# Kernel tuning notes

Measured on AMD Instinct MI355X. Metric: run time of the kernel, lower is better.

The kernel has to match this reference:

```python
import jax, jax.numpy as jnp
import numpy as np

N_HEAD = 8
HID = 64
IN_DIM = 512
OUT_DIM = 512


def setup_inputs() -> dict:
    key = jax.random.key(0)
    ks = jax.random.split(key, 12)
    B, LQ, LK = 2, 2048, 2048
    stdv = 1.0 / np.sqrt(HID)
    inp = {
        "q": jax.random.normal(ks[0], (B, LQ, IN_DIM), jnp.float32),
        "k": jax.random.normal(ks[1], (B, LK, IN_DIM), jnp.float32),
        "v": jax.random.normal(ks[2], (B, LK, IN_DIM), jnp.float32),
        # linear params stored as (in, out); torch Linear applies x @ W.T + b,
        # we store pre-transposed weights so y = x @ W + b is the same math.
        "Wq": jax.random.normal(ks[3], (IN_DIM, N_HEAD * HID), jnp.float32) * 0.02,
        "bq": jnp.zeros((N_HEAD * HID,), jnp.float32),
        "Wk": jax.random.normal(ks[4], (IN_DIM, N_HEAD * HID), jnp.float32) * 0.02,
        "bk": jnp.zeros((N_HEAD * HID,), jnp.float32),
        "Wv": jax.random.normal(ks[5], (IN_DIM, N_HEAD * HID), jnp.float32) * 0.02,
        "bv": jnp.zeros((N_HEAD * HID,), jnp.float32),
        # mlp-method scoring vector, uniform(-stdv, stdv), length 2*hidden
        "w_score": jax.random.uniform(ks[6], (2 * HID,), jnp.float32, -stdv, stdv),
        "Wd": jax.random.normal(ks[7], (N_HEAD * HID, OUT_DIM), jnp.float32) * 0.02,
        "bd": jnp.zeros((OUT_DIM,), jnp.float32),
    }
    return inp


def reference(q, k, v, Wq, bq, Wk, bk, Wv, bv, w_score, Wd, bd):
    B, Lq, _ = q.shape
    Lk = k.shape[1]
    # project and split heads -> (n_head, B, L, hid), matching torch's
    # permute(2,0,1,3).view(n_head*B, L, hid) layout
    qx = (q @ Wq + bq).reshape(B, Lq, N_HEAD, HID).transpose(2, 0, 1, 3)
    kx = (k @ Wk + bk).reshape(B, Lk, N_HEAD, HID).transpose(2, 0, 1, 3)
    vx = (v @ Wv + bv).reshape(B, Lk, N_HEAD, HID).transpose(2, 0, 1, 3)
    # 'mlp' additive attention: tanh(cat(q_i, k_j) . w) == tanh(q_i.w1 + k_j.w2)
    # computed as a broadcast sum instead of materializing the concat tensor
    w1, w2 = w_score[:HID], w_score[HID:]
    qw = qx @ w1  # (n_head, B, Lq)
    kw = kx @ w2  # (n_head, B, Lk)
    score = jnp.tanh(qw[..., :, None] + kw[..., None, :])  # (n_head, B, Lq, Lk)
    score = jax.nn.softmax(score, axis=-1)
    out_head = jnp.einsum('hbqk,hbkd->hbqd', score, vx)  # (n_head, B, Lq, hid)
    # torch: split along head*batch dim then cat along features -> head-major concat
    out = out_head.transpose(1, 2, 0, 3).reshape(B, Lq, N_HEAD * HID)
    output = out @ Wd + bd  # dropout is identity in eval
    score_flat = score.reshape(N_HEAD * B, Lq, Lk)
    return output, score_flat
```

## Files before the change

### kernel.cpp

```cpp
#include <hip/hip_runtime.h>
#include <math.h>

#define B_  2
#define L_  2048
#define D_  512
#define NH_ 8
#define HD_ 64

typedef __attribute__((ext_vector_type(8))) short short8;
typedef __attribute__((ext_vector_type(4))) float f32x4;

__device__ __forceinline__ float ex2(float x) {
#if __has_builtin(__builtin_amdgcn_exp2f)
    return __builtin_amdgcn_exp2f(x);
#else
    return exp2f(x);
#endif
}
__device__ __forceinline__ float rcp_(float x) {
#if __has_builtin(__builtin_amdgcn_rcpf)
    return __builtin_amdgcn_rcpf(x);
#else
    return 1.0f / x;
#endif
}

__device__ __forceinline__ float fast_e(float x) {
    float z  = ex2(x * 2.885390082f);
    float th = 1.0f - 2.0f * rcp_(z + 1.0f);
    return ex2(th * 1.4426950408889634f);
}

__device__ __forceinline__ unsigned int f2bf(float x) {
    unsigned int u = __float_as_uint(x);
    u += 0x7fffu + ((u >> 16) & 1u);
    return u >> 16;
}
__device__ __forceinline__ unsigned int pk2(float lo, float hi) {
    return f2bf(lo) | (f2bf(hi) << 16);
}

__global__ void k_prep(const float* __restrict__ Wq, const float* __restrict__ bq,
                       const float* __restrict__ Wk, const float* __restrict__ bk,
                       const float* __restrict__ wsc,
                       float* __restrict__ wqwT, float* __restrict__ wkwT,
                       float* __restrict__ bqw, float* __restrict__ bkw) {
    __shared__ float w[HD_];
    int which = blockIdx.x >> 1;
    int half  = blockIdx.x & 1;
    const float* W  = which ? Wk : Wq;
    const float* bb = which ? bk : bq;
    float* WT = which ? wkwT : wqwT;
    float* bo = which ? bkw  : bqw;
    if (threadIdx.x < HD_) w[threadIdx.x] = wsc[which * HD_ + threadIdx.x];
    __syncthreads();
    int r = half * 256 + threadIdx.x;
    for (int h = 0; h < NH_; ++h) {
        float s = 0.f;
        #pragma unroll 8
        for (int d = 0; d < HD_; ++d) s += W[r * D_ + h * HD_ + d] * w[d];
        WT[h * D_ + r] = s;
    }
    if (half == 0 && threadIdx.x < NH_) {
        int h = threadIdx.x;
        float s = 0.f;
        for (int d = 0; d < HD_; ++d) s += bb[h * HD_ + d] * w[d];
        bo[h] = s;
    }
}

__global__ void k_wconv(const float* __restrict__ Wv, const float* __restrict__ Wd,
                        unsigned short* __restrict__ WvF,
                        unsigned short* __restrict__ WdFh,
                        unsigned short* __restrict__ WdFl) {
    int id = blockIdx.x * 256 + threadIdx.x;
    int lane = id & 63;
    int kb = (id >> 6) & 15;
    int nf = id >> 10;
    int l15 = lane & 15, lg = lane >> 4;
    int n = nf * 16 + l15;
    int k0 = kb * 32 + lg * 4;
    size_t base = ((size_t)(nf * 16 + kb) * 64 + lane) * 8;
    if (blockIdx.y == 0) {
        #pragma unroll
        for (int j = 0; j < 8; ++j) {
            int k = k0 + (j & 3) + 16 * (j >> 2);
            WvF[base + j] = (unsigned short)f2bf(Wv[(size_t)k * 512 + n]);
        }
    } else {
        #pragma unroll
        for (int j = 0; j < 8; ++j) {
            int k = k0 + (j & 3) + 16 * (j >> 2);
            float x = Wd[(size_t)k * 512 + n];
            unsigned int h = f2bf(x);
            float hf = __uint_as_float(h << 16);
            WdFh[base + j] = (unsigned short)h;
            WdFl[base + j] = (unsigned short)f2bf(x - hf);
        }
    }
}

__global__ void k_qwkw(const float* __restrict__ q, const float* __restrict__ k,
                       const float* __restrict__ wqwT, const float* __restrict__ wkwT,
                       const float* __restrict__ bqw, const float* __restrict__ bkw,
                       float* __restrict__ qw, float* __restrict__ kw) {
    int wid  = blockIdx.x * 4 + (threadIdx.x >> 6);
    int lane = threadIdx.x & 63;
    int sel  = wid >= 4096;
    int row  = wid & 4095;
    const float* src = sel ? k : q;
    const float* WT  = sel ? wkwT : wqwT;
    const float* bo  = sel ? bkw : bqw;
    float* dst = sel ? kw : qw;
    float4 va = *(const float4*)(src + (size_t)row * D_ + lane * 4);
    float4 vb = *(const float4*)(src + (size_t)row * D_ + 256 + lane * 4);
    float res[NH_];
    #pragma unroll
    for (int h = 0; h < NH_; ++h) {
        float4 wa = *(const float4*)(WT + h * D_ + lane * 4);
        float4 wb = *(const float4*)(WT + h * D_ + 256 + lane * 4);
        float s = va.x*wa.x + va.y*wa.y + va.z*wa.z + va.w*wa.w
                + vb.x*wb.x + vb.y*wb.y + vb.z*wb.z + vb.w*wb.w;
        #pragma unroll
        for (int off = 32; off; off >>= 1) s += __shfl_xor(s, off);
        res[h] = s + bo[h];
    }
    if (lane == 0) {
        #pragma unroll
        for (int h = 0; h < NH_; ++h) dst[h * 4096 + row] = res[h];
    }
}

__global__ __launch_bounds__(256) void k_mmA(const float* __restrict__ A,
                                             const short8* __restrict__ BF,
                                             const float* __restrict__ bias,
                                             unsigned short* __restrict__ vxg) {
    int m0 = blockIdx.x * 64;
    int n0q = blockIdx.y * 4;
    int tid = threadIdx.x;
    int w = tid >> 6, lane = tid & 63;
    int l15 = lane & 15, lg = lane >> 4;
    f32x4 acc[4];
    #pragma unroll
    for (int j = 0; j < 4; ++j) acc[j] = (f32x4){0.f, 0.f, 0.f, 0.f};

    const float* a0 = A + (size_t)(m0 + w * 16 + l15) * 512 + lg * 4;

    float4 clo = *(const float4*)(a0);
    float4 chi = *(const float4*)(a0 + 16);
    short8 cb[4];
    #pragma unroll
    for (int nf = 0; nf < 4; ++nf) cb[nf] = BF[(size_t)(n0q + nf) * 16 * 64 + lane];

    for (int kb = 0; kb < 16; ++kb) {
        float4 lo = clo, hi = chi;
        short8 b0 = cb[0], b1 = cb[1], b2 = cb[2], b3 = cb[3];
        if (kb < 15) {
            clo = *(const float4*)(a0 + (kb + 1) * 32);
            chi = *(const float4*)(a0 + (kb + 1) * 32 + 16);
            #pragma unroll
            for (int nf = 0; nf < 4; ++nf)
                cb[nf] = BF[((size_t)(n0q + nf) * 16 + kb + 1) * 64 + lane];
        }
        union { unsigned int u[4]; short8 s; } af;
        asm("v_cvt_pk_bf16_f32 %0, %1, %2" : "=v"(af.u[0]) : "v"(lo.x), "v"(lo.y));
        asm("v_cvt_pk_bf16_f32 %0, %1, %2" : "=v"(af.u[1]) : "v"(lo.z), "v"(lo.w));
        asm("v_cvt_pk_bf16_f32 %0, %1, %2" : "=v"(af.u[2]) : "v"(hi.x), "v"(hi.y));
        asm("v_cvt_pk_bf16_f32 %0, %1, %2" : "=v"(af.u[3]) : "v"(hi.z), "v"(hi.w));
        acc[0] = __builtin_amdgcn_mfma_f32_16x16x32_bf16(af.s, b0, acc[0], 0, 0, 0);
        acc[1] = __builtin_amdgcn_mfma_f32_16x16x32_bf16(af.s, b1, acc[1], 0, 0, 0);
        acc[2] = __builtin_amdgcn_mfma_f32_16x16x32_bf16(af.s, b2, acc[2], 0, 0, 0);
        acc[3] = __builtin_amdgcn_mfma_f32_16x16x32_bf16(af.s, b3, acc[3], 0, 0, 0);
    }
    int m = m0 + w * 16 + lg * 4;
    int b = m >> 11, kk = m & 2047;
    int kblk = kk >> 5, base32 = kk & 31;
    int ie0 = 4 * (base32 >> 4);
    int lvsel = 16 * ((base32 >> 2) & 3);
    #pragma unroll
    for (int nf = 0; nf < 4; ++nf) {
        int n = (n0q + nf) * 16 + l15;
        float bvv = bias[n];
        int h = n >> 6, dt = (n >> 4) & 3, ncol = n & 15;
        int lane_v = ncol + lvsel;
        size_t ad = ((((size_t)((h * 2 + b) * 64 + kblk)) * 4 + dt) * 64 + lane_v) * 8 + ie0;
        uint2 pkt;
        pkt.x = pk2(acc[nf][0] + bvv, acc[nf][1] + bvv);
        pkt.y = pk2(acc[nf][2] + bvv, acc[nf][3] + bvv);
        *(uint2*)(vxg + ad) = pkt;
    }
}

__global__ __launch_bounds__(256) void k_mmB(const float* __restrict__ A,
                                             const short8* __restrict__ BFh,
                                             const short8* __restrict__ BFl,
                                             const float* __restrict__ bias,
                                             float* __restrict__ C) {
    int m0 = blockIdx.x * 64;
    int n0q = blockIdx.y * 4;
    int tid = threadIdx.x;
    int w = tid >> 6, lane = tid & 63;
    int l15 = lane & 15, lg = lane >> 4;
    f32x4 acc[4];
    #pragma unroll
    for (int j = 0; j < 4; ++j) acc[j] = (f32x4){0.f, 0.f, 0.f, 0.f};

    const float* a0 = A + (size_t)(m0 + w * 16 + l15) * 512 + lg * 4;

    float4 clo = *(const float4*)(a0);
    float4 chi = *(const float4*)(a0 + 16);

    for (int kb = 0; kb < 16; ++kb) {
        float4 lo = clo, hi = chi;
        if (kb < 15) {
            clo = *(const float4*)(a0 + (kb + 1) * 32);
            chi = *(const float4*)(a0 + (kb + 1) * 32 + 16);
        }
        union { unsigned int u[4]; short8 s; } ah, al;
        {
            float xs[8] = {lo.x, lo.y, lo.z, lo.w, hi.x, hi.y, hi.z, hi.w};
            unsigned int hu[8]; float lf[8];
            #pragma unroll
            for (int j = 0; j < 8; ++j) {
                hu[j] = f2bf(xs[j]);
                lf[j] = xs[j] - __uint_as_float(hu[j] << 16);
            }
            #pragma unroll
            for (int j = 0; j < 4; ++j) {
                ah.u[j] = hu[2 * j] | (hu[2 * j + 1] << 16);
                al.u[j] = pk2(lf[2 * j], lf[2 * j + 1]);
            }
        }
        #pragma unroll
        for (int nf = 0; nf < 4; ++nf) {
            size_t bi = ((size_t)(n0q + nf) * 16 + kb) * 64 + lane;
            short8 bh = BFh[bi];
            short8 bl = BFl[bi];
            acc[nf] = __builtin_amdgcn_mfma_f32_16x16x32_bf16(ah.s, bh, acc[nf], 0, 0, 0);
            acc[nf] = __builtin_amdgcn_mfma_f32_16x16x32_bf16(al.s, bh, acc[nf], 0, 0, 0);
            acc[nf] = __builtin_amdgcn_mfma_f32_16x16x32_bf16(ah.s, bl, acc[nf], 0, 0, 0);
        }
    }
    #pragma unroll
    for (int nf = 0; nf < 4; ++nf) {
        int n = (n0q + nf) * 16 + l15;
        float bdv = bias[n];
        #pragma unroll
        for (int r = 0; r < 4; ++r) {
            int m = m0 + w * 16 + lg * 4 + r;
            C[(size_t)m * 512 + n] = acc[nf][r] + bdv;
        }
    }
}

__global__ __launch_bounds__(512, 4) void k_main(const float* __restrict__ qw,
                                                 const float* __restrict__ kw,
                                                 const short8* __restrict__ vgs,
                                                 float* __restrict__ att,
                                                 float* __restrict__ rsum_o) {
    int hb  = blockIdx.y;
    int q0  = blockIdx.x * 64;
    int tid = threadIdx.x;
    int w   = tid >> 6;
    int wq  = w & 3;
    int kh  = w >> 2;
    int lane = tid & 63;
    int l15 = lane & 15, lg = lane >> 4;

    __shared__ float kws[2048];
    __shared__ float red[4][16][68];

    *(float4*)&kws[tid * 4] = *(const float4*)(kw + hb * 2048 + tid * 4);
    __syncthreads();

    float qwv = qw[hb * 2048 + q0 + wq * 16 + l15];
    const short8* bp = vgs + (size_t)hb * 16384 + lane;

    f32x4 acc0 = {0,0,0,0}, acc1 = {0,0,0,0}, acc2 = {0,0,0,0}, acc3 = {0,0,0,0};
    f32x4 accs = {0,0,0,0};
    union { unsigned int u[4]; short8 s; } ones_;
    ones_.u[0] = 0x3f803f80u; ones_.u[1] = 0x3f803f80u;
    ones_.u[2] = 0x3f803f80u; ones_.u[3] = 0x3f803f80u;

    int kb0 = kh * 32;
    const short8* pb = bp + (size_t)kb0 * 256;
    short8 cb0 = pb[0], cb1 = pb[64], cb2 = pb[128], cb3 = pb[192];
    float4 ckw0 = *(const float4*)&kws[kb0 * 32 + lg * 4];
    float4 ckw1 = *(const float4*)&kws[kb0 * 32 + lg * 4 + 16];

    for (int i = 0; i < 32; ++i) {
        short8 b0 = cb0, b1 = cb1, b2 = cb2, b3 = cb3;
        float4 kw0 = ckw0, kw1 = ckw1;
        if (i < 31) {
            const short8* nb = bp + (size_t)(kb0 + i + 1) * 256;
            cb0 = nb[0]; cb1 = nb[64]; cb2 = nb[128]; cb3 = nb[192];
            int nk = (kb0 + i + 1) * 32 + lg * 4;
            ckw0 = *(const float4*)&kws[nk];
            ckw1 = *(const float4*)&kws[nk + 16];
        }
        float e0 = fast_e(qwv + kw0.x), e1 = fast_e(qwv + kw0.y);
        float e2 = fast_e(qwv + kw0.z), e3 = fast_e(qwv + kw0.w);
        float e4 = fast_e(qwv + kw1.x), e5 = fast_e(qwv + kw1.y);
        float e6 = fast_e(qwv + kw1.z), e7 = fast_e(qwv + kw1.w);
        union { unsigned int u[4]; short8 s; } af;
        asm("v_cvt_pk_bf16_f32 %0, %1, %2" : "=v"(af.u[0]) : "v"(e0), "v"(e1));
        asm("v_cvt_pk_bf16_f32 %0, %1, %2" : "=v"(af.u[1]) : "v"(e2), "v"(e3));
        asm("v_cvt_pk_bf16_f32 %0, %1, %2" : "=v"(af.u[2]) : "v"(e4), "v"(e5));
        asm("v_cvt_pk_bf16_f32 %0, %1, %2" : "=v"(af.u[3]) : "v"(e6), "v"(e7));
        acc0 = __builtin_amdgcn_mfma_f32_16x16x32_bf16(af.s, b0, acc0, 0, 0, 0);
        acc1 = __builtin_amdgcn_mfma_f32_16x16x32_bf16(af.s, b1, acc1, 0, 0, 0);
        acc2 = __builtin_amdgcn_mfma_f32_16x16x32_bf16(af.s, b2, acc2, 0, 0, 0);
        acc3 = __builtin_amdgcn_mfma_f32_16x16x32_bf16(af.s, b3, acc3, 0, 0, 0);
        accs = __builtin_amdgcn_mfma_f32_16x16x32_bf16(af.s, ones_.s, accs, 0, 0, 0);
    }

    if (kh == 1) {
        #define WR_(dt, accv) \
            red[wq][lg * 4 + 0][dt * 16 + l15] = accv[0]; \
            red[wq][lg * 4 + 1][dt * 16 + l15] = accv[1]; \
            red[wq][lg * 4 + 2][dt * 16 + l15] = accv[2]; \
            red[wq][lg * 4 + 3][dt * 16 + l15] = accv[3];
        WR_(0, acc0) WR_(1, acc1) WR_(2, acc2) WR_(3, acc3)
        #undef WR_
        if (l15 == 0) {
            red[wq][lg * 4 + 0][64] = accs[0];
            red[wq][lg * 4 + 1][64] = accs[1];
            red[wq][lg * 4 + 2][64] = accs[2];
            red[wq][lg * 4 + 3][64] = accs[3];
        }
    }
    __syncthreads();
    if (kh == 0) {
        #define RD_(dt, accv) \
            accv[0] += red[wq][lg * 4 + 0][dt * 16 + l15]; \
            accv[1] += red[wq][lg * 4 + 1][dt * 16 + l15]; \
            accv[2] += red[wq][lg * 4 + 2][dt * 16 + l15]; \
            accv[3] += red[wq][lg * 4 + 3][dt * 16 + l15];
        RD_(0, acc0) RD_(1, acc1) RD_(2, acc2) RD_(3, acc3)
        #undef RD_
        float rs0 = 1.0f / (accs[0] + red[wq][lg * 4 + 0][64]);
        float rs1 = 1.0f / (accs[1] + red[wq][lg * 4 + 1][64]);
        float rs2 = 1.0f / (accs[2] + red[wq][lg * 4 + 2][64]);
        float rs3 = 1.0f / (accs[3] + red[wq][lg * 4 + 3][64]);
        if (l15 == 0) {
            rsum_o[hb * 2048 + q0 + wq * 16 + lg * 4 + 0] = rs0;
            rsum_o[hb * 2048 + q0 + wq * 16 + lg * 4 + 1] = rs1;
            rsum_o[hb * 2048 + q0 + wq * 16 + lg * 4 + 2] = rs2;
            rsum_o[hb * 2048 + q0 + wq * 16 + lg * 4 + 3] = rs3;
        }
        int b_ = hb & 1, h = hb >> 1;
        float* ab = att + ((size_t)(b_ * 2048 + q0 + wq * 16 + lg * 4)) * 512 + h * 64 + l15;
        #define ST_(dt, accv) \
            ab[0 * 512 + dt * 16] = accv[0] * rs0; \
            ab[1 * 512 + dt * 16] = accv[1] * rs1; \
            ab[2 * 512 + dt * 16] = accv[2] * rs2; \
            ab[3 * 512 + dt * 16] = accv[3] * rs3;
        ST_(0, acc0) ST_(1, acc1) ST_(2, acc2) ST_(3, acc3)
        #undef ST_
    }
}

__global__ void k_score(const float* __restrict__ qw, const float* __restrict__ kw,
                        const float* __restrict__ rsum, float* __restrict__ score) {
    int hb = blockIdx.y;
    int tid = threadIdx.x;
    __shared__ float kws[2048];
    *(float4*)&kws[tid * 8]     = *(const float4*)(kw + hb * 2048 + tid * 8);
    *(float4*)&kws[tid * 8 + 4] = *(const float4*)(kw + hb * 2048 + tid * 8 + 4);
    __syncthreads();
    int rl  = tid >> 5;
    int t32 = tid & 31;
    int q = blockIdx.x * 8 + rl;
    float qwv = qw[hb * 2048 + q];
    float rs  = rsum[hb * 2048 + q];
    float* out = score + ((size_t)(hb * 2048 + q)) * 2048;
    #pragma unroll
    for (int i = 0; i < 16; ++i) {
        int k = i * 128 + t32 * 4;
        float4 o;
        o.x = fast_e(qwv + kws[k + 0]) * rs;
        o.y = fast_e(qwv + kws[k + 1]) * rs;
        o.z = fast_e(qwv + kws[k + 2]) * rs;
        o.w = fast_e(qwv + kws[k + 3]) * rs;
        *(float4*)(out + k) = o;
    }
}

extern "C" void kernel_launch(void* const* d_in, const int* in_sizes, int n_in,
                              void* d_out, int out_size, void* d_ws, size_t ws_size,
                              hipStream_t stream) {
    (void)in_sizes; (void)n_in; (void)out_size; (void)ws_size;
    const float* q   = (const float*)d_in[0];
    const float* k   = (const float*)d_in[1];
    const float* v   = (const float*)d_in[2];
    const float* Wq  = (const float*)d_in[3];
    const float* bq  = (const float*)d_in[4];
    const float* Wk  = (const float*)d_in[5];
    const float* bk  = (const float*)d_in[6];
    const float* Wv  = (const float*)d_in[7];
    const float* bv  = (const float*)d_in[8];
    const float* wsc = (const float*)d_in[9];
    const float* Wd  = (const float*)d_in[10];
    const float* bd  = (const float*)d_in[11];

    float* out   = (float*)d_out;
    float* score = out + (size_t)B_ * L_ * D_;

    float* ws    = (float*)d_ws;
    float* wqwT  = ws;
    float* wkwT  = ws + 4096;
    float* bqw   = ws + 8192;
    float* bkw   = ws + 8256;
    float* qw    = ws + 8704;
    float* kw    = ws + 41472;
    float* rsum  = ws + 74240;
    float* vxg   = ws + 107008;
    float* att   = ws + 1155584;
    float* WvF   = ws + 3252736;
    float* WdFh  = ws + 3383808;
    float* WdFl  = ws + 3514880;

    k_prep<<<dim3(4), dim3(256), 0, stream>>>(Wq, bq, Wk, bk, wsc, wqwT, wkwT, bqw, bkw);
    k_wconv<<<dim3(128, 2), dim3(256), 0, stream>>>(Wv, Wd,
        (unsigned short*)WvF, (unsigned short*)WdFh, (unsigned short*)WdFl);
    k_qwkw<<<dim3(2048), dim3(256), 0, stream>>>(q, k, wqwT, wkwT, bqw, bkw, qw, kw);
    k_mmA<<<dim3(64, 8), dim3(256), 0, stream>>>(v, (const short8*)WvF, bv,
        (unsigned short*)vxg);
    k_main<<<dim3(32, 16), dim3(512), 0, stream>>>(qw, kw, (const short8*)vxg, att, rsum);
    k_score<<<dim3(256, 16), dim3(256), 0, stream>>>(qw, kw, rsum, score);
    k_mmB<<<dim3(64, 8), dim3(256), 0, stream>>>(att, (const short8*)WdFh,
        (const short8*)WdFl, bd, out);
}
```

Before: 160.1 us.

## Merge independent kernels into horizontally fused launches with interleaved block roles

```diff
diff --git a/kernel.cpp b/kernel.cpp
--- a/kernel.cpp
+++ b/kernel.cpp
@@ -40,215 +40,169 @@
     return f2bf(lo) | (f2bf(hi) << 16);
 }
 
-__global__ void k_prep(const float* __restrict__ Wq, const float* __restrict__ bq,
-                       const float* __restrict__ Wk, const float* __restrict__ bk,
-                       const float* __restrict__ wsc,
-                       float* __restrict__ wqwT, float* __restrict__ wkwT,
-                       float* __restrict__ bqw, float* __restrict__ bkw) {
-    __shared__ float w[HD_];
-    int which = blockIdx.x >> 1;
-    int half  = blockIdx.x & 1;
-    const float* W  = which ? Wk : Wq;
-    const float* bb = which ? bk : bq;
-    float* WT = which ? wkwT : wqwT;
-    float* bo = which ? bkw  : bqw;
-    if (threadIdx.x < HD_) w[threadIdx.x] = wsc[which * HD_ + threadIdx.x];
-    __syncthreads();
-    int r = half * 256 + threadIdx.x;
-    for (int h = 0; h < NH_; ++h) {
-        float s = 0.f;
-        #pragma unroll 8
-        for (int d = 0; d < HD_; ++d) s += W[r * D_ + h * HD_ + d] * w[d];
-        WT[h * D_ + r] = s;
-    }
-    if (half == 0 && threadIdx.x < NH_) {
-        int h = threadIdx.x;
-        float s = 0.f;
-        for (int d = 0; d < HD_; ++d) s += bb[h * HD_ + d] * w[d];
-        bo[h] = s;
-    }
-}
-
-__global__ void k_wconv(const float* __restrict__ Wv, const float* __restrict__ Wd,
-                        unsigned short* __restrict__ WvF,
-                        unsigned short* __restrict__ WdFh,
-                        unsigned short* __restrict__ WdFl) {
-    int id = blockIdx.x * 256 + threadIdx.x;
-    int lane = id & 63;
-    int kb = (id >> 6) & 15;
-    int nf = id >> 10;
-    int l15 = lane & 15, lg = lane >> 4;
-    int n = nf * 16 + l15;
-    int k0 = kb * 32 + lg * 4;
-    size_t base = ((size_t)(nf * 16 + kb) * 64 + lane) * 8;
-    if (blockIdx.y == 0) {
-        #pragma unroll
-        for (int j = 0; j < 8; ++j) {
-            int k = k0 + (j & 3) + 16 * (j >> 2);
-            WvF[base + j] = (unsigned short)f2bf(Wv[(size_t)k * 512 + n]);
+__global__ __launch_bounds__(256) void k_pw(const float* __restrict__ Wq,
+                                            const float* __restrict__ bq,
+                                            const float* __restrict__ Wk,
+                                            const float* __restrict__ bk,
+                                            const float* __restrict__ wsc,
+                                            float* __restrict__ wqwT,
+                                            float* __restrict__ wkwT,
+                                            float* __restrict__ bqw,
+                                            float* __restrict__ bkw,
+                                            const float* __restrict__ Wv,
+                                            const float* __restrict__ Wd,
+                                            unsigned short* __restrict__ WvF,
+                                            unsigned short* __restrict__ WdFh,
+                                            unsigned short* __restrict__ WdFl) {
+    if (blockIdx.x < 4) {
+        __shared__ float w[HD_];
+        int which = blockIdx.x >> 1;
+        int half  = blockIdx.x & 1;
+        const float* W  = which ? Wk : Wq;
+        const float* bb = which ? bk : bq;
+        float* WT = which ? wkwT : wqwT;
+        float* bo = which ? bkw  : bqw;
+        if (threadIdx.x < HD_) w[threadIdx.x] = wsc[which * HD_ + threadIdx.x];
+        __syncthreads();
+        int r = half * 256 + threadIdx.x;
+        for (int h = 0; h < NH_; ++h) {
+            float s = 0.f;
+            #pragma unroll 8
+            for (int d = 0; d < HD_; ++d) s += W[r * D_ + h * HD_ + d] * w[d];
+            WT[h * D_ + r] = s;
+        }
+        if (half == 0 && threadIdx.x < NH_) {
+            int h = threadIdx.x;
+            float s = 0.f;
+            for (int d = 0; d < HD_; ++d) s += bb[h * HD_ + d] * w[d];
+            bo[h] = s;
         }
     } else {
-        #pragma unroll
-        for (int j = 0; j < 8; ++j) {
-            int k = k0 + (j & 3) + 16 * (j >> 2);
-            float x = Wd[(size_t)k * 512 + n];
-            unsigned int h = f2bf(x);
-            float hf = __uint_as_float(h << 16);
-            WdFh[base + j] = (unsigned short)h;
-            WdFl[base + j] = (unsigned short)f2bf(x - hf);
-        }
-    }
-}
-
-__global__ void k_qwkw(const float* __restrict__ q, const float* __restrict__ k,
-                       const float* __restrict__ wqwT, const float* __restrict__ wkwT,
-                       const float* __restrict__ bqw, const float* __restrict__ bkw,
-                       float* __restrict__ qw, float* __restrict__ kw) {
-    int wid  = blockIdx.x * 4 + (threadIdx.x >> 6);
-    int lane = threadIdx.x & 63;
-    int sel  = wid >= 4096;
-    int row  = wid & 4095;
-    const float* src = sel ? k : q;
-    const float* WT  = sel ? wkwT : wqwT;
-    const float* bo  = sel ? bkw : bqw;
-    float* dst = sel ? kw : qw;
-    float4 va = *(const float4*)(src + (size_t)row * D_ + lane * 4);
-    float4 vb = *(const float4*)(src + (size_t)row * D_ + 256 + lane * 4);
-    float res[NH_];
-    #pragma unroll
-    for (int h = 0; h < NH_; ++h) {
-        float4 wa = *(const float4*)(WT + h * D_ + lane * 4);
-        float4 wb = *(const float4*)(WT + h * D_ + 256 + lane * 4);
-        float s = va.x*wa.x + va.y*wa.y + va.z*wa.z + va.w*wa.w
-                + vb.x*wb.x + vb.y*wb.y + vb.z*wb.z + vb.w*wb.w;
-        #pragma unroll
-        for (int off = 32; off; off >>= 1) s += __shfl_xor(s, off);
-        res[h] = s + bo[h];
-    }
-    if (lane == 0) {
-        #pragma unroll
-        for (int h = 0; h < NH_; ++h) dst[h * 4096 + row] = res[h];
-    }
-}
-
-__global__ __launch_bounds__(256) void k_mmA(const float* __restrict__ A,
-                                             const short8* __restrict__ BF,
-                                             const float* __restrict__ bias,
-                                             unsigned short* __restrict__ vxg) {
-    int m0 = blockIdx.x * 64;
-    int n0q = blockIdx.y * 4;
+        int id = (blockIdx.x - 4) * 256 + threadIdx.x;
+        int wy = id >> 15;
+        int wid = id & 32767;
+        int lane = wid & 63;
+        int kb = (wid >> 6) & 15;
+        int nf = wid >> 10;
+        int l15 = lane & 15, lg = lane >> 4;
+        int n = nf * 16 + l15;
+        int k0 = kb * 32 + lg * 4;
+        size_t base = ((size_t)(nf * 16 + kb) * 64 + lane) * 8;
+        if (wy == 0) {
+            #pragma unroll
+            for (int j = 0; j < 8; ++j) {
+                int k = k0 + (j & 3) + 16 * (j >> 2);
+                WvF[base + j] = (unsigned short)f2bf(Wv[(size_t)k * 512 + n]);
+            }
+        } else {
+            #pragma unroll
+            for (int j = 0; j < 8; ++j) {
+                int k = k0 + (j & 3) + 16 * (j >> 2);
+                float x = Wd[(size_t)k * 512 + n];
+                unsigned int h = f2bf(x);
+                float hf = __uint_as_float(h << 16);
+                WdFh[base + j] = (unsigned short)h;
+                WdFl[base + j] = (unsigned short)f2bf(x - hf);
+            }
+        }
+    }
+}
+
+__global__ __launch_bounds__(256) void k_qm(const float* __restrict__ q,
+                                            const float* __restrict__ k,
+                                            const float* __restrict__ wqwT,
+                                            const float* __restrict__ wkwT,
+                                            const float* __restrict__ bqw,
+                                            const float* __restrict__ bkw,
+                                            float* __restrict__ qw,
+                                            float* __restrict__ kw,
+                                            const float* __restrict__ A,
+                                            const short8* __restrict__ BF,
+                                            const float* __restrict__ bias,
+                                            unsigned short* __restrict__ vxg) {
+    int bx = blockIdx.x;
     int tid = threadIdx.x;
-    int w = tid >> 6, lane = tid & 63;
-    int l15 = lane & 15, lg = lane >> 4;
-    f32x4 acc[4];
-    #pragma unroll
-    for (int j = 0; j < 4; ++j) acc[j] = (f32x4){0.f, 0.f, 0.f, 0.f};
-
-    const float* a0 = A + (size_t)(m0 + w * 16 + l15) * 512 + lg * 4;
-
-    float4 clo = *(const float4*)(a0);
-    float4 chi = *(const float4*)(a0 + 16);
-    short8 cb[4];
-    #pragma unroll
-    for (int nf = 0; nf < 4; ++nf) cb[nf] = BF[(size_t)(n0q + nf) * 16 * 64 + lane];
-
-    for (int kb = 0; kb < 16; ++kb) {
-        float4 lo = clo, hi = chi;
-        short8 b0 = cb[0], b1 = cb[1], b2 = cb[2], b3 = cb[3];
-        if (kb < 15) {
-            clo = *(const float4*)(a0 + (kb + 1) * 32);
-            chi = *(const float4*)(a0 + (kb + 1) * 32 + 16);
-            #pragma unroll
-            for (int nf = 0; nf < 4; ++nf)
-                cb[nf] = BF[((size_t)(n0q + nf) * 16 + kb + 1) * 64 + lane];
-        }
-        union { unsigned int u[4]; short8 s; } af;
-        asm("v_cvt_pk_bf16_f32 %0, %1, %2" : "=v"(af.u[0]) : "v"(lo.x), "v"(lo.y));
-        asm("v_cvt_pk_bf16_f32 %0, %1, %2" : "=v"(af.u[1]) : "v"(lo.z), "v"(lo.w));
-        asm("v_cvt_pk_bf16_f32 %0, %1, %2" : "=v"(af.u[2]) : "v"(hi.x), "v"(hi.y));
-        asm("v_cvt_pk_bf16_f32 %0, %1, %2" : "=v"(af.u[3]) : "v"(hi.z), "v"(hi.w));
-        acc[0] = __builtin_amdgcn_mfma_f32_16x16x32_bf16(af.s, b0, acc[0], 0, 0, 0);
-        acc[1] = __builtin_amdgcn_mfma_f32_16x16x32_bf16(af.s, b1, acc[1], 0, 0, 0);
-        acc[2] = __builtin_amdgcn_mfma_f32_16x16x32_bf16(af.s, b2, acc[2], 0, 0, 0);
-        acc[3] = __builtin_amdgcn_mfma_f32_16x16x32_bf16(af.s, b3, acc[3], 0, 0, 0);
-    }
-    int m = m0 + w * 16 + lg * 4;
-    int b = m >> 11, kk = m & 2047;
-    int kblk = kk >> 5, base32 = kk & 31;
-    int ie0 = 4 * (base32 >> 4);
-    int lvsel = 16 * ((base32 >> 2) & 3);
-    #pragma unroll
-    for (int nf = 0; nf < 4; ++nf) {
-        int n = (n0q + nf) * 16 + l15;
-        float bvv = bias[n];
-        int h = n >> 6, dt = (n >> 4) & 3, ncol = n & 15;
-        int lane_v = ncol + lvsel;
-        size_t ad = ((((size_t)((h * 2 + b) * 64 + kblk)) * 4 + dt) * 64 + lane_v) * 8 + ie0;
-        uint2 pkt;
-        pkt.x = pk2(acc[nf][0] + bvv, acc[nf][1] + bvv);
-        pkt.y = pk2(acc[nf][2] + bvv, acc[nf][3] + bvv);
-        *(uint2*)(vxg + ad) = pkt;
-    }
-}
-
-__global__ __launch_bounds__(256) void k_mmB(const float* __restrict__ A,
-                                             const short8* __restrict__ BFh,
-                                             const short8* __restrict__ BFl,
-                                             const float* __restrict__ bias,
-                                             float* __restrict__ C) {
-    int m0 = blockIdx.x * 64;
-    int n0q = blockIdx.y * 4;
-    int tid = threadIdx.x;
-    int w = tid >> 6, lane = tid & 63;
-    int l15 = lane & 15, lg = lane >> 4;
-    f32x4 acc[4];
-    #pragma unroll
-    for (int j = 0; j < 4; ++j) acc[j] = (f32x4){0.f, 0.f, 0.f, 0.f};
-
-    const float* a0 = A + (size_t)(m0 + w * 16 + l15) * 512 + lg * 4;
-
-    float4 clo = *(const float4*)(a0);
-    float4 chi = *(const float4*)(a0 + 16);
-
-    for (int kb = 0; kb < 16; ++kb) {
-        float4 lo = clo, hi = chi;
-        if (kb < 15) {
-            clo = *(const float4*)(a0 + (kb + 1) * 32);
-            chi = *(const float4*)(a0 + (kb + 1) * 32 + 16);
-        }
-        union { unsigned int u[4]; short8 s; } ah, al;
-        {
-            float xs[8] = {lo.x, lo.y, lo.z, lo.w, hi.x, hi.y, hi.z, hi.w};
-            unsigned int hu[8]; float lf[8];
-            #pragma unroll
-            for (int j = 0; j < 8; ++j) {
-                hu[j] = f2bf(xs[j]);
-                lf[j] = xs[j] - __uint_as_float(hu[j] << 16);
-            }
-            #pragma unroll
-            for (int j = 0; j < 4; ++j) {
-                ah.u[j] = hu[2 * j] | (hu[2 * j + 1] << 16);
-                al.u[j] = pk2(lf[2 * j], lf[2 * j + 1]);
-            }
-        }
+    if (bx % 5 == 0) {
+        int mb = bx / 5;
+        int m0 = (mb & 63) * 64;
+        int n0q = (mb >> 6) * 4;
+        int w = tid >> 6, lane = tid & 63;
+        int l15 = lane & 15, lg = lane >> 4;
+        f32x4 acc[4];
+        #pragma unroll
+        for (int j = 0; j < 4; ++j) acc[j] = (f32x4){0.f, 0.f, 0.f, 0.f};
+
+        const float* a0 = A + (size_t)(m0 + w * 16 + l15) * 512 + lg * 4;
+
+        float4 clo = *(const float4*)(a0);
+        float4 chi = *(const float4*)(a0 + 16);
+        short8 cb[4];
+        #pragma unroll
+        for (int nf = 0; nf < 4; ++nf) cb[nf] = BF[(size_t)(n0q + nf) * 16 * 64 + lane];
+
+        for (int kb = 0; kb < 16; ++kb) {
+            float4 lo = clo, hi = chi;
+            short8 b0 = cb[0], b1 = cb[1], b2 = cb[2], b3 = cb[3];
+            if (kb < 15) {
+                clo = *(const float4*)(a0 + (kb + 1) * 32);
+                chi = *(const float4*)(a0 + (kb + 1) * 32 + 16);
+                #pragma unroll
+                for (int nf = 0; nf < 4; ++nf)
+                    cb[nf] = BF[((size_t)(n0q + nf) * 16 + kb + 1) * 64 + lane];
+            }
+            union { unsigned int u[4]; short8 s; } af;
+            asm("v_cvt_pk_bf16_f32 %0, %1, %2" : "=v"(af.u[0]) : "v"(lo.x), "v"(lo.y));
+            asm("v_cvt_pk_bf16_f32 %0, %1, %2" : "=v"(af.u[1]) : "v"(lo.z), "v"(lo.w));
+            asm("v_cvt_pk_bf16_f32 %0, %1, %2" : "=v"(af.u[2]) : "v"(hi.x), "v"(hi.y));
+            asm("v_cvt_pk_bf16_f32 %0, %1, %2" : "=v"(af.u[3]) : "v"(hi.z), "v"(hi.w));
+            acc[0] = __builtin_amdgcn_mfma_f32_16x16x32_bf16(af.s, b0, acc[0], 0, 0, 0);
+            acc[1] = __builtin_amdgcn_mfma_f32_16x16x32_bf16(af.s, b1, acc[1], 0, 0, 0);
+            acc[2] = __builtin_amdgcn_mfma_f32_16x16x32_bf16(af.s, b2, acc[2], 0, 0, 0);
+            acc[3] = __builtin_amdgcn_mfma_f32_16x16x32_bf16(af.s, b3, acc[3], 0, 0, 0);
+        }
+        int m = m0 + w * 16 + lg * 4;
+        int b = m >> 11, kk = m & 2047;
+        int kblk = kk >> 5, base32 = kk & 31;
+        int ie0 = 4 * (base32 >> 4);
+        int lvsel = 16 * ((base32 >> 2) & 3);
         #pragma unroll
         for (int nf = 0; nf < 4; ++nf) {
-            size_t bi = ((size_t)(n0q + nf) * 16 + kb) * 64 + lane;
-            short8 bh = BFh[bi];
-            short8 bl = BFl[bi];
-            acc[nf] = __builtin_amdgcn_mfma_f32_16x16x32_bf16(ah.s, bh, acc[nf], 0, 0, 0);
-            acc[nf] = __builtin_amdgcn_mfma_f32_16x16x32_bf16(al.s, bh, acc[nf], 0, 0, 0);
-            acc[nf] = __builtin_amdgcn_mfma_f32_16x16x32_bf16(ah.s, bl, acc[nf], 0, 0, 0);
-        }
-    }
-    #pragma unroll
-    for (int nf = 0; nf < 4; ++nf) {
-        int n = (n0q + nf) * 16 + l15;
-        float bdv = bias[n];
-        #pragma unroll
-        for (int r = 0; r < 4; ++r) {
-            int m = m0 + w * 16 + lg * 4 + r;
-            C[(size_t)m * 512 + n] = acc[nf][r] + bdv;
+            int n = (n0q + nf) * 16 + l15;
+            float bvv = bias[n];
+            int h = n >> 6, dt = (n >> 4) & 3, ncol = n & 15;
+            int lane_v = ncol + lvsel;
+            size_t ad = ((((size_t)((h * 2 + b) * 64 + kblk)) * 4 + dt) * 64 + lane_v) * 8 + ie0;
+            uint2 pkt;
+            pkt.x = pk2(acc[nf][0] + bvv, acc[nf][1] + bvv);
+            pkt.y = pk2(acc[nf][2] + bvv, acc[nf][3] + bvv);
+            *(uint2*)(vxg + ad) = pkt;
+        }
+    } else {
+        int qb = bx - bx / 5 - 1;
+        int wid  = qb * 4 + (tid >> 6);
+        int lane = tid & 63;
+        int sel  = wid >= 4096;
+        int row  = wid & 4095;
+        const float* src = sel ? k : q;
+        const float* WT  = sel ? wkwT : wqwT;
+        const float* bo  = sel ? bkw : bqw;
+        float* dst = sel ? kw : qw;
+        float4 va = *(const float4*)(src + (size_t)row * D_ + lane * 4);
+        float4 vb = *(const float4*)(src + (size_t)row * D_ + 256 + lane * 4);
+        float res[NH_];
+        #pragma unroll
+        for (int h = 0; h < NH_; ++h) {
+            float4 wa = *(const float4*)(WT + h * D_ + lane * 4);
+            float4 wb = *(const float4*)(WT + h * D_ + 256 + lane * 4);
+            float s = va.x*wa.x + va.y*wa.y + va.z*wa.z + va.w*wa.w
+                    + vb.x*wb.x + vb.y*wb.y + vb.z*wb.z + vb.w*wb.w;
+            #pragma unroll
+            for (int off = 32; off; off >>= 1) s += __shfl_xor(s, off);
+            res[h] = s + bo[h];
+        }
+        if (lane == 0) {
+            #pragma unroll
+            for (int h = 0; h < NH_; ++h) dst[h * 4096 + row] = res[h];
         }
     }
 }
@@ -360,29 +314,97 @@
     }
 }
 
-__global__ void k_score(const float* __restrict__ qw, const float* __restrict__ kw,
-                        const float* __restrict__ rsum, float* __restrict__ score) {
-    int hb = blockIdx.y;
+__global__ __launch_bounds__(256) void k_sm(const float* __restrict__ qw,
+                                            const float* __restrict__ kw,
+                                            const float* __restrict__ rsum,
+                                            float* __restrict__ score,
+                                            const float* __restrict__ A,
+                                            const short8* __restrict__ BFh,
+                                            const short8* __restrict__ BFl,
+                                            const float* __restrict__ bias,
+                                            float* __restrict__ C) {
+    __shared__ float kws[2048];
+    int bx  = blockIdx.x;
     int tid = threadIdx.x;
-    __shared__ float kws[2048];
-    *(float4*)&kws[tid * 8]     = *(const float4*)(kw + hb * 2048 + tid * 8);
-    *(float4*)&kws[tid * 8 + 4] = *(const float4*)(kw + hb * 2048 + tid * 8 + 4);
-    __syncthreads();
-    int rl  = tid >> 5;
-    int t32 = tid & 31;
-    int q = blockIdx.x * 8 + rl;
-    float qwv = qw[hb * 2048 + q];
-    float rs  = rsum[hb * 2048 + q];
-    float* out = score + ((size_t)(hb * 2048 + q)) * 2048;
-    #pragma unroll
-    for (int i = 0; i < 16; ++i) {
-        int k = i * 128 + t32 * 4;
-        float4 o;
-        o.x = fast_e(qwv + kws[k + 0]) * rs;
-        o.y = fast_e(qwv + kws[k + 1]) * rs;
-        o.z = fast_e(qwv + kws[k + 2]) * rs;
-        o.w = fast_e(qwv + kws[k + 3]) * rs;
-        *(float4*)(out + k) = o;
+    if (bx % 9 == 0) {
+        int mb = bx / 9;
+        int m0 = (mb & 63) * 64;
+        int n0q = (mb >> 6) * 4;
+        int w = tid >> 6, lane = tid & 63;
+        int l15 = lane & 15, lg = lane >> 4;
+        f32x4 acc[4];
+        #pragma unroll
+        for (int j = 0; j < 4; ++j) acc[j] = (f32x4){0.f, 0.f, 0.f, 0.f};
+
+        const float* a0 = A + (size_t)(m0 + w * 16 + l15) * 512 + lg * 4;
+
+        float4 clo = *(const float4*)(a0);
+        float4 chi = *(const float4*)(a0 + 16);
+
+        for (int kb = 0; kb < 16; ++kb) {
+            float4 lo = clo, hi = chi;
+            if (kb < 15) {
+                clo = *(const float4*)(a0 + (kb + 1) * 32);
+                chi = *(const float4*)(a0 + (kb + 1) * 32 + 16);
+            }
+            union { unsigned int u[4]; short8 s; } ah, al;
+            {
+                float xs[8] = {lo.x, lo.y, lo.z, lo.w, hi.x, hi.y, hi.z, hi.w};
+                unsigned int hu[8]; float lf[8];
+                #pragma unroll
+                for (int j = 0; j < 8; ++j) {
+                    hu[j] = f2bf(xs[j]);
+                    lf[j] = xs[j] - __uint_as_float(hu[j] << 16);
+                }
+                #pragma unroll
+                for (int j = 0; j < 4; ++j) {
+                    ah.u[j] = hu[2 * j] | (hu[2 * j + 1] << 16);
+                    al.u[j] = pk2(lf[2 * j], lf[2 * j + 1]);
+                }
+            }
+            #pragma unroll
+            for (int nf = 0; nf < 4; ++nf) {
+                size_t bi = ((size_t)(n0q + nf) * 16 + kb) * 64 + lane;
+                short8 bh = BFh[bi];
+                short8 bl = BFl[bi];
+                acc[nf] = __builtin_amdgcn_mfma_f32_16x16x32_bf16(ah.s, bh, acc[nf], 0, 0, 0);
+                acc[nf] = __builtin_amdgcn_mfma_f32_16x16x32_bf16(al.s, bh, acc[nf], 0, 0, 0);
+                acc[nf] = __builtin_amdgcn_mfma_f32_16x16x32_bf16(ah.s, bl, acc[nf], 0, 0, 0);
+            }
+        }
+        #pragma unroll
+        for (int nf = 0; nf < 4; ++nf) {
+            int n = (n0q + nf) * 16 + l15;
+            float bdv = bias[n];
+            #pragma unroll
+            for (int r = 0; r < 4; ++r) {
+                int m = m0 + w * 16 + lg * 4 + r;
+                C[(size_t)m * 512 + n] = acc[nf][r] + bdv;
+            }
+        }
+    } else {
+        int sb = bx - bx / 9 - 1;
+        int hb = sb >> 8;
+        int qx = sb & 255;
+        *(float4*)&kws[tid * 8]     = *(const float4*)(kw + hb * 2048 + tid * 8);
+        *(float4*)&kws[tid * 8 + 4] = *(const float4*)(kw + hb * 2048 + tid * 8 + 4);
+        __syncthreads();
+        int rl  = tid >> 5;
+        int t32 = tid & 31;
+        int qrow = qx * 8 + rl;
+        float qwv = qw[hb * 2048 + qrow];
+        float rs  = rsum[hb * 2048 + qrow];
+        float* outp = score + ((size_t)(hb * 2048 + qrow)) * 2048;
+        #pragma unroll
+        for (int i = 0; i < 16; ++i) {
+            int kk = i * 128 + t32 * 4;
+            float4 o;
+            o.x = fast_e(qwv + kws[kk + 0]) * rs;
+            o.y = fast_e(qwv + kws[kk + 1]) * rs;
+            o.z = fast_e(qwv + kws[kk + 2]) * rs;
+            o.w = fast_e(qwv + kws[kk + 3]) * rs;
+            *(float4*)(outp + kk) = o;
+        }
     }
 }
 
@@ -420,14 +442,13 @@
     float* WdFh  = ws + 3383808;
     float* WdFl  = ws + 3514880;
 
-    k_prep<<<dim3(4), dim3(256), 0, stream>>>(Wq, bq, Wk, bk, wsc, wqwT, wkwT, bqw, bkw);
-    k_wconv<<<dim3(128, 2), dim3(256), 0, stream>>>(Wv, Wd,
+    k_pw<<<dim3(260), dim3(256), 0, stream>>>(Wq, bq, Wk, bk, wsc,
+        wqwT, wkwT, bqw, bkw, Wv, Wd,
         (unsigned short*)WvF, (unsigned short*)WdFh, (unsigned short*)WdFl);
-    k_qwkw<<<dim3(2048), dim3(256), 0, stream>>>(q, k, wqwT, wkwT, bqw, bkw, qw, kw);
-    k_mmA<<<dim3(64, 8), dim3(256), 0, stream>>>(v, (const short8*)WvF, bv,
-        (unsigned short*)vxg);
-    k_main<<<dim3(32, 16), dim3(512), 0, stream>>>(qw, kw, (const short8*)vxg, att, rsum);
-    k_score<<<dim3(256, 16), dim3(256), 0, stream>>>(qw, kw, rsum, score);
-    k_mmB<<<dim3(64, 8), dim3(256), 0, stream>>>(att, (const short8*)WdFh,
-        (const short8*)WdFl, bd, out);
-}
+    k_qm<<<dim3(2560), dim3(256), 0, stream>>>(q, k, wqwT, wkwT, bqw, bkw,
+        qw, kw, v, (const short8*)WvF, bv, (unsigned short*)vxg);
+    k_main<<<dim3(32, 16), dim3(512), 0, stream>>>(qw, kw, (const short8*)vxg,
+        att, rsum);
+    k_sm<<<dim3(4608), dim3(256), 0, stream>>>(qw, kw, rsum, score,
+        att, (const short8*)WdFh, (const short8*)WdFl, bd, out);
+}
```

New measurement: 155.4 us. -2.9%, faster.
